# Optimization experiments

Measured on AMD Instinct MI355X. Metric: run time of the kernel, lower is better.

## Reference

```python
import jax, jax.numpy as jnp
import numpy as np

B = 4096
D_FULL, D_T1, D_T2 = 1024, 512, 512
N_SPEC, N_SHARED = 4, 4
HID, OUT = 512, 256


def _expert_params(key, n_experts, d_in):
    k1, k2, k3, k4 = jax.random.split(key, 4)
    s1 = 1.0 / np.sqrt(d_in)
    s2 = 1.0 / np.sqrt(HID)
    return {
        'W1': jax.random.uniform(k1, (n_experts, d_in, HID), jnp.float32, -s1, s1),
        'b1': jax.random.uniform(k2, (n_experts, HID), jnp.float32, -s1, s1),
        'W2': jax.random.uniform(k3, (n_experts, HID, OUT), jnp.float32, -s2, s2),
        'b2': jax.random.uniform(k4, (n_experts, OUT), jnp.float32, -s2, s2),
    }


def setup_inputs() -> dict:
    key = jax.random.key(0)
    ks = jax.random.split(key, 12)
    x_full = jax.random.normal(ks[0], (B, D_FULL), jnp.float32)
    x_task1 = jax.random.normal(ks[1], (B, D_T1), jnp.float32)
    x_task2 = jax.random.normal(ks[2], (B, D_T2), jnp.float32)
    ps = _expert_params(ks[3], N_SHARED, D_FULL)
    p1 = _expert_params(ks[4], N_SPEC, D_T1)
    p2 = _expert_params(ks[5], N_SPEC, D_T2)
    sg = 1.0 / np.sqrt(D_FULL)
    s1 = 1.0 / np.sqrt(D_T1)
    s2 = 1.0 / np.sqrt(D_T2)
    return {
        'x_full': x_full, 'x_task1': x_task1, 'x_task2': x_task2,
        'sh_W1': ps['W1'], 'sh_b1': ps['b1'], 'sh_W2': ps['W2'], 'sh_b2': ps['b2'],
        't1_W1': p1['W1'], 't1_b1': p1['b1'], 't1_W2': p1['W2'], 't1_b2': p1['b2'],
        't2_W1': p2['W1'], 't2_b1': p2['b1'], 't2_W2': p2['W2'], 't2_b2': p2['b2'],
        'gsh_W': jax.random.uniform(ks[6], (D_FULL, 2 * N_SPEC + N_SHARED), jnp.float32, -sg, sg),
        'gsh_b': jax.random.uniform(ks[7], (2 * N_SPEC + N_SHARED,), jnp.float32, -sg, sg),
        'g1_W': jax.random.uniform(ks[8], (D_T1, N_SPEC + N_SHARED), jnp.float32, -s1, s1),
        'g1_b': jax.random.uniform(ks[9], (N_SPEC + N_SHARED,), jnp.float32, -s1, s1),
        'g2_W': jax.random.uniform(ks[10], (D_T2, N_SPEC + N_SHARED), jnp.float32, -s2, s2),
        'g2_b': jax.random.uniform(ks[11], (N_SPEC + N_SHARED,), jnp.float32, -s2, s2),
    }


def _experts(x, W1, b1, W2, b2):
    # x: [B, D]; W1: [E, D, H] -> out [E, B, OUT]
    h = jax.nn.relu(jnp.einsum('bd,edh->ebh', x, W1) + b1[:, None, :])
    return jax.nn.relu(jnp.einsum('ebh,eho->ebo', h, W2) + b2[:, None, :])


def reference(x_full, x_task1, x_task2,
              sh_W1, sh_b1, sh_W2, sh_b2,
              t1_W1, t1_b1, t1_W2, t1_b2,
              t2_W1, t2_b1, t2_W2, t2_b2,
              gsh_W, gsh_b, g1_W, g1_b, g2_W, g2_b):
    eo_shared = _experts(x_full, sh_W1, sh_b1, sh_W2, sh_b2)    # [Es, B, OUT]
    eo_t1 = _experts(x_task1, t1_W1, t1_b1, t1_W2, t1_b2)       # [Et, B, OUT]
    eo_t2 = _experts(x_task2, t2_W1, t2_b1, t2_W2, t2_b2)       # [Et, B, OUT]

    g1 = jax.nn.softmax(x_task1 @ g1_W + g1_b, axis=1)          # [B, Et+Es]
    out1 = jnp.einsum('ebc,be->bc', jnp.concatenate([eo_t1, eo_shared], axis=0), g1)

    g2 = jax.nn.softmax(x_task2 @ g2_W + g2_b, axis=1)
    out2 = jnp.einsum('ebc,be->bc', jnp.concatenate([eo_t2, eo_shared], axis=0), g2)

    gsh = jax.nn.softmax(x_full @ gsh_W + gsh_b, axis=1)        # [B, 2Et+Es]
    out_sh = jnp.einsum('ebc,be->bc', jnp.concatenate([eo_t1, eo_t2, eo_shared], axis=0), gsh)

    return (out_sh, out1, out2)
```

## Files before the change

kernel.cpp:

```cpp
#include <hip/hip_runtime.h>

typedef unsigned short u16;
typedef __attribute__((ext_vector_type(8))) short short8;
typedef __attribute__((ext_vector_type(4))) float f32x4;

#define GL2LDS16(src, dst) __builtin_amdgcn_global_load_lds( \
    (const __attribute__((address_space(1))) void*)(src),    \
    (__attribute__((address_space(3))) void*)(dst), 16, 0, 0)

__device__ __forceinline__ u16 f2bf(float f) {
  union { float f; unsigned u; } v; v.f = f;
  unsigned r = v.u + 0x7fffu + ((v.u >> 16) & 1u);
  return (u16)(r >> 16);
}
__device__ __forceinline__ float bf2f(u16 h) {
  union { unsigned u; float f; } v; v.u = ((unsigned)h) << 16; return v.f;
}

__global__ void k_gates_cvt(const float* __restrict__ xf, const float* __restrict__ x1,
                            const float* __restrict__ x2,
                            const float* __restrict__ gshW, const float* __restrict__ gshB,
                            const float* __restrict__ g1W, const float* __restrict__ g1B,
                            const float* __restrict__ g2W, const float* __restrict__ g2B,
                            u16* __restrict__ xfb, u16* __restrict__ x1b, u16* __restrict__ x2b,
                            float* __restrict__ gsh, float* __restrict__ g1o,
                            float* __restrict__ g2o) {
  const int b = blockIdx.x, lane = threadIdx.x;
  float s[12];
#pragma unroll
  for (int j = 0; j < 12; ++j) s[j] = 0.f;
  {
    const float* xr = xf + (size_t)b * 1024;
    u16* xw = xfb + (size_t)b * 1024;
    for (int k = lane; k < 1024; k += 64) {
      float v = xr[k];
      xw[k] = f2bf(v);
      const float* wr = gshW + (size_t)k * 12;
#pragma unroll
      for (int j = 0; j < 12; ++j) s[j] += v * wr[j];
    }
  }
  float u[8], w[8];
#pragma unroll
  for (int j = 0; j < 8; ++j) { u[j] = 0.f; w[j] = 0.f; }
  {
    const float* xr1 = x1 + (size_t)b * 512;
    const float* xr2 = x2 + (size_t)b * 512;
    u16* xw1 = x1b + (size_t)b * 512;
    u16* xw2 = x2b + (size_t)b * 512;
    for (int k = lane; k < 512; k += 64) {
      float v1 = xr1[k], v2 = xr2[k];
      xw1[k] = f2bf(v1); xw2[k] = f2bf(v2);
      const float* w1r = g1W + (size_t)k * 8;
      const float* w2r = g2W + (size_t)k * 8;
#pragma unroll
      for (int j = 0; j < 8; ++j) { u[j] += v1 * w1r[j]; w[j] += v2 * w2r[j]; }
    }
  }
#pragma unroll
  for (int off = 32; off >= 1; off >>= 1) {
#pragma unroll
    for (int j = 0; j < 12; ++j) s[j] += __shfl_xor(s[j], off, 64);
#pragma unroll
    for (int j = 0; j < 8; ++j) { u[j] += __shfl_xor(u[j], off, 64); w[j] += __shfl_xor(w[j], off, 64); }
  }
  if (lane == 0) {
    float m = -1e30f, tot = 0.f;
#pragma unroll
    for (int j = 0; j < 12; ++j) { s[j] += gshB[j]; m = fmaxf(m, s[j]); }
#pragma unroll
    for (int j = 0; j < 12; ++j) { s[j] = __expf(s[j] - m); tot += s[j]; }
    float inv = 1.f / tot;
#pragma unroll
    for (int j = 0; j < 12; ++j) gsh[(size_t)b * 12 + j] = s[j] * inv;
    m = -1e30f; tot = 0.f;
#pragma unroll
    for (int j = 0; j < 8; ++j) { u[j] += g1B[j]; m = fmaxf(m, u[j]); }
#pragma unroll
    for (int j = 0; j < 8; ++j) { u[j] = __expf(u[j] - m); tot += u[j]; }
    inv = 1.f / tot;
#pragma unroll
    for (int j = 0; j < 8; ++j) g1o[(size_t)b * 8 + j] = u[j] * inv;
    m = -1e30f; tot = 0.f;
#pragma unroll
    for (int j = 0; j < 8; ++j) { w[j] += g2B[j]; m = fmaxf(m, w[j]); }
#pragma unroll
    for (int j = 0; j < 8; ++j) { w[j] = __expf(w[j] - m); tot += w[j]; }
    inv = 1.f / tot;
#pragma unroll
    for (int j = 0; j < 8; ++j) g2o[(size_t)b * 8 + j] = w[j] * inv;
  }
}

struct TD { const float* src; u16* dst; int lgTps; int lgNtx; int R; int C; int tileBase; };
struct TArgs { TD d[6]; };

__global__ void k_transpose_all(TArgs ta) {
  __shared__ float tile[32][33];
  const int x = blockIdx.x;
  int di = 0;
#pragma unroll
  for (int i = 1; i < 6; ++i)
    if (x >= ta.d[i].tileBase) di = i;
  TD d = ta.d[di];
  const int local = x - d.tileBase;
  const int slice = local >> d.lgTps;
  const int ti = local & ((1 << d.lgTps) - 1);
  const int tx = ti & ((1 << d.lgNtx) - 1);
  const int ty = ti >> d.lgNtx;
  const float* src = d.src + (size_t)slice * d.R * d.C;
  u16* dst = d.dst + (size_t)slice * d.R * d.C;
  const int c0 = tx * 32, r0 = ty * 32;
  const int ttx = threadIdx.x, tty = threadIdx.y;
#pragma unroll
  for (int i = tty; i < 32; i += 8)
    tile[i][ttx] = src[(size_t)(r0 + i) * d.C + (c0 + ttx)];
  __syncthreads();
#pragma unroll
  for (int i = tty; i < 32; i += 8)
    dst[(size_t)(c0 + i) * d.R + (r0 + ttx)] = f2bf(tile[ttx][i]);
}

struct GemmDesc {
  const u16* A;
  const u16* BT;
  const float* bias;
  u16* C;
  int K;
  int N;
  int T;
};
struct GemmArgs { GemmDesc d[12]; };

#define BARR __builtin_amdgcn_s_barrier()
#define WAITL0                                                   \
  {                                                              \
    asm volatile("s_waitcnt lgkmcnt(0)" ::: "memory");           \
    __builtin_amdgcn_sched_barrier(0);                           \
  }
#define WAITV0 asm volatile("s_waitcnt vmcnt(0)" ::: "memory")

__global__ __launch_bounds__(512, 4) void k_gemm128(GemmArgs args) {
  __shared__ __align__(16) u16 As[2 * 128 * 32];
  __shared__ __align__(16) u16 Bs[2 * 256 * 32];

  GemmDesc g = args.d[blockIdx.y];
  const int K = g.K, N = g.N, T = g.T;
  const int ntN = N >> 8;
  const int bx = blockIdx.x;
  const int nt = bx & (ntN - 1);
  const int bt = (ntN == 2) ? (bx >> 1) : bx;
  const int row0 = bt << 7;
  const int col0 = nt << 8;

  const int tid = threadIdx.x;
  const int lane = tid & 63;
  const int wid = tid >> 6;
  const int wm = wid & 1;
  const int wn = wid >> 1;
  const int lrow = lane & 15;
  const int lkq = lane >> 4;

  const int csw = (lkq ^ (lrow & 3)) * 16;
  int aoff[4], boff[4];
#pragma unroll
  for (int mi = 0; mi < 4; ++mi) aoff[mi] = (wm * 64 + mi * 16 + lrow) * 64 + csw;
#pragma unroll
  for (int ni = 0; ni < 4; ++ni) boff[ni] = (wn * 64 + ni * 16 + lrow) * 64 + csw;

  const int ar = tid >> 2;
  const int acs = (tid & 3) ^ (ar & 3);
  const u16* aSrc = g.A + (size_t)(row0 + ar) * K + acs * 8;
  const int br0 = tid >> 2;
  const int bc0 = (tid & 3) ^ (br0 & 3);
  const u16* bSrc0 = g.BT + (size_t)(col0 + br0) * K + bc0 * 8;
  const int br1 = 128 + (tid >> 2);
  const int bc1 = (tid & 3) ^ (br1 & 3);
  const u16* bSrc1 = g.BT + (size_t)(col0 + br1) * K + bc1 * 8;

  auto STAGE = [&](int buf, int t) {
    GL2LDS16(aSrc + (size_t)t * 32, &As[buf * 4096 + tid * 8]);
    GL2LDS16(bSrc0 + (size_t)t * 32, &Bs[buf * 8192 + tid * 8]);
    GL2LDS16(bSrc1 + (size_t)t * 32, &Bs[buf * 8192 + 4096 + tid * 8]);
  };

  f32x4 acc[4][4];
#pragma unroll
  for (int m = 0; m < 4; ++m)
#pragma unroll
    for (int n = 0; n < 4; ++n)
      acc[m][n] = (f32x4){0.f, 0.f, 0.f, 0.f};

  STAGE(0, 0);
  WAITV0;
  BARR;

  for (int t = 0; t < T; ++t) {
    const int buf = t & 1;
    const char* Ab = (const char*)As + buf * 8192;
    const char* Bb = (const char*)Bs + buf * 16384;
    short8 a0, a1, b[4];
#pragma unroll
    for (int ni = 0; ni < 4; ++ni) b[ni] = *(const short8*)(Bb + boff[ni]);
    a0 = *(const short8*)(Ab + aoff[0]);
    a1 = *(const short8*)(Ab + aoff[1]);
    if (t + 1 < T) STAGE(buf ^ 1, t + 1);
    WAITL0;
    __builtin_amdgcn_s_setprio(1);
#pragma unroll
    for (int ni = 0; ni < 4; ++ni) {
      acc[0][ni] = __builtin_amdgcn_mfma_f32_16x16x32_bf16(a0, b[ni], acc[0][ni], 0, 0, 0);
      acc[1][ni] = __builtin_amdgcn_mfma_f32_16x16x32_bf16(a1, b[ni], acc[1][ni], 0, 0, 0);
    }
    __builtin_amdgcn_s_setprio(0);
    a0 = *(const short8*)(Ab + aoff[2]);
    a1 = *(const short8*)(Ab + aoff[3]);
    WAITL0;
    __builtin_amdgcn_s_setprio(1);
#pragma unroll
    for (int ni = 0; ni < 4; ++ni) {
      acc[2][ni] = __builtin_amdgcn_mfma_f32_16x16x32_bf16(a0, b[ni], acc[2][ni], 0, 0, 0);
      acc[3][ni] = __builtin_amdgcn_mfma_f32_16x16x32_bf16(a1, b[ni], acc[3][ni], 0, 0, 0);
    }
    __builtin_amdgcn_s_setprio(0);
    WAITV0;
    BARR;
  }

#pragma unroll
  for (int ni = 0; ni < 4; ++ni) {
    const int gc = col0 + wn * 64 + ni * 16 + lrow;
    const float bv = g.bias[gc];
#pragma unroll
    for (int mi = 0; mi < 4; ++mi) {
      const int gr = row0 + wm * 64 + mi * 16 + lkq * 4;
#pragma unroll
      for (int j = 0; j < 4; ++j) {
        float o = fmaxf(acc[mi][ni][j] + bv, 0.f);
        g.C[(size_t)(gr + j) * N + gc] = f2bf(o);
      }
    }
  }
}

__global__ void k_reduce(const u16* __restrict__ OutB, const float* __restrict__ gsh,
                         const float* __restrict__ g1, const float* __restrict__ g2,
                         float* __restrict__ out) {
  int t = blockIdx.x * 256 + threadIdx.x;
  int b = t >> 5;
  int c0 = (t & 31) << 3;
  float wsh[12], w1[8], w2[8];
#pragma unroll
  for (int j = 0; j < 12; ++j) wsh[j] = gsh[(size_t)b * 12 + j];
#pragma unroll
  for (int j = 0; j < 8; ++j) { w1[j] = g1[(size_t)b * 8 + j]; w2[j] = g2[(size_t)b * 8 + j]; }
  float ash[8] = {0, 0, 0, 0, 0, 0, 0, 0};
  float a1[8] = {0, 0, 0, 0, 0, 0, 0, 0};
  float a2[8] = {0, 0, 0, 0, 0, 0, 0, 0};
#pragma unroll
  for (int e = 0; e < 12; ++e) {
    short8 v = *(const short8*)&OutB[((size_t)e * 4096 + b) * 256 + c0];
    float f[8];
#pragma unroll
    for (int i = 0; i < 8; ++i) f[i] = bf2f((u16)v[i]);
#pragma unroll
    for (int i = 0; i < 8; ++i) ash[i] += wsh[e] * f[i];
    if (e < 4) {
#pragma unroll
      for (int i = 0; i < 8; ++i) a1[i] += w1[e] * f[i];
    } else if (e < 8) {
#pragma unroll
      for (int i = 0; i < 8; ++i) a2[i] += w2[e - 4] * f[i];
    } else {
#pragma unroll
      for (int i = 0; i < 8; ++i) a1[i] += w1[e - 4] * f[i];
#pragma unroll
      for (int i = 0; i < 8; ++i) a2[i] += w2[e - 4] * f[i];
    }
  }
  size_t base = (size_t)b * 256 + c0;
  float4* o;
  o = (float4*)(out + base);
  o[0] = make_float4(ash[0], ash[1], ash[2], ash[3]);
  o[1] = make_float4(ash[4], ash[5], ash[6], ash[7]);
  o = (float4*)(out + 4096ull * 256 + base);
  o[0] = make_float4(a1[0], a1[1], a1[2], a1[3]);
  o[1] = make_float4(a1[4], a1[5], a1[6], a1[7]);
  o = (float4*)(out + 2ull * 4096 * 256 + base);
  o[0] = make_float4(a2[0], a2[1], a2[2], a2[3]);
  o[1] = make_float4(a2[4], a2[5], a2[6], a2[7]);
}

extern "C" void kernel_launch(void* const* d_in, const int* in_sizes, int n_in,
                              void* d_out, int out_size, void* d_ws, size_t ws_size,
                              hipStream_t stream) {
  const float* x_full = (const float*)d_in[0];
  const float* x_t1 = (const float*)d_in[1];
  const float* x_t2 = (const float*)d_in[2];
  const float* sh_W1 = (const float*)d_in[3];
  const float* sh_b1 = (const float*)d_in[4];
  const float* sh_W2 = (const float*)d_in[5];
  const float* sh_b2 = (const float*)d_in[6];
  const float* t1_W1 = (const float*)d_in[7];
  const float* t1_b1 = (const float*)d_in[8];
  const float* t1_W2 = (const float*)d_in[9];
  const float* t1_b2 = (const float*)d_in[10];
  const float* t2_W1 = (const float*)d_in[11];
  const float* t2_b1 = (const float*)d_in[12];
  const float* t2_W2 = (const float*)d_in[13];
  const float* t2_b2 = (const float*)d_in[14];
  const float* gsh_W = (const float*)d_in[15];
  const float* gsh_b = (const float*)d_in[16];
  const float* g1_W = (const float*)d_in[17];
  const float* g1_b = (const float*)d_in[18];
  const float* g2_W = (const float*)d_in[19];
  const float* g2_b = (const float*)d_in[20];

  char* ws = (char*)d_ws;
  size_t off = 0;
  auto alloc = [&](size_t bytes) -> void* {
    void* p = ws + off;
    off += (bytes + 255) & ~(size_t)255;
    return p;
  };
  u16* xf_b = (u16*)alloc(4096ull * 1024 * 2);
  u16* x1_b = (u16*)alloc(4096ull * 512 * 2);
  u16* x2_b = (u16*)alloc(4096ull * 512 * 2);
  u16* w1t_t1 = (u16*)alloc(4ull * 512 * 512 * 2);
  u16* w1t_t2 = (u16*)alloc(4ull * 512 * 512 * 2);
  u16* w1t_sh = (u16*)alloc(4ull * 512 * 1024 * 2);
  u16* w2t = (u16*)alloc(12ull * 256 * 512 * 2);
  u16* H = (u16*)alloc(12ull * 4096 * 512 * 2);
  u16* OutB = (u16*)alloc(12ull * 4096 * 256 * 2);
  float* gshv = (float*)alloc(4096ull * 12 * 4);
  float* g1v = (float*)alloc(4096ull * 8 * 4);
  float* g2v = (float*)alloc(4096ull * 8 * 4);

  k_gates_cvt<<<4096, 64, 0, stream>>>(x_full, x_t1, x_t2, gsh_W, gsh_b, g1_W, g1_b, g2_W, g2_b,
                                       xf_b, x1_b, x2_b, gshv, g1v, g2v);

  TArgs ta;
  ta.d[0] = TD{t1_W1, w1t_t1, 8, 4, 512, 512, 0};
  ta.d[1] = TD{t2_W1, w1t_t2, 8, 4, 512, 512, 1024};
  ta.d[2] = TD{sh_W1, w1t_sh, 9, 4, 1024, 512, 2048};
  ta.d[3] = TD{t1_W2, w2t, 7, 3, 512, 256, 4096};
  ta.d[4] = TD{t2_W2, w2t + 4ull * 256 * 512, 7, 3, 512, 256, 4608};
  ta.d[5] = TD{sh_W2, w2t + 8ull * 256 * 512, 7, 3, 512, 256, 5120};
  k_transpose_all<<<5632, dim3(32, 8), 0, stream>>>(ta);

  GemmArgs ga1;
  for (int e = 0; e < 4; ++e) {
    ga1.d[e] = GemmDesc{xf_b, w1t_sh + (size_t)e * 512 * 1024, sh_b1 + e * 512,
                        H + (size_t)(8 + e) * 4096 * 512, 1024, 512, 32};
    ga1.d[4 + e] = GemmDesc{x1_b, w1t_t1 + (size_t)e * 512 * 512, t1_b1 + e * 512,
                            H + (size_t)e * 4096 * 512, 512, 512, 16};
    ga1.d[8 + e] = GemmDesc{x2_b, w1t_t2 + (size_t)e * 512 * 512, t2_b1 + e * 512,
                            H + (size_t)(4 + e) * 4096 * 512, 512, 512, 16};
  }
  k_gemm128<<<dim3(64, 12), 512, 0, stream>>>(ga1);

  GemmArgs ga2;
  for (int e = 0; e < 12; ++e) {
    const float* bias = (e < 4) ? (t1_b2 + e * 256)
                      : (e < 8) ? (t2_b2 + (e - 4) * 256)
                                : (sh_b2 + (e - 8) * 256);
    ga2.d[e] = GemmDesc{H + (size_t)e * 4096 * 512, w2t + (size_t)e * 256 * 512, bias,
                        OutB + (size_t)e * 4096 * 256, 512, 256, 16};
  }
  k_gemm128<<<dim3(32, 12), 512, 0, stream>>>(ga2);

  k_reduce<<<512, 256, 0, stream>>>(OutB, gshv, g1v, g2v, (float*)d_out);
}
```

Measured before the change: 108.0 us.

## Load GEMM A operand directly from global into registers, keep B in LDS

The A tile no longer goes through shared memory. Each wave now reads its A fragments straight from global memory into registers, one step ahead, while B tiles stay double-buffered in LDS through async global-to-LDS loads. The vmcnt waits are made partial so the register prefetch of A overlaps the B staging, the four MFMA row groups are merged into one pass, and the LDS swizzle is changed to XOR with (row>>1). This halves LDS traffic and footprint, at the cost of more global load instructions per wave, since A rows are reread by the four waves sharing wm, and more registers to hold the prefetched A.

```diff
diff --git a/kernel.cpp b/kernel.cpp
--- a/kernel.cpp
+++ b/kernel.cpp
@@ -138,10 +138,13 @@
     asm volatile("s_waitcnt lgkmcnt(0)" ::: "memory");           \
     __builtin_amdgcn_sched_barrier(0);                           \
   }
-#define WAITV0 asm volatile("s_waitcnt vmcnt(0)" ::: "memory")
-
-__global__ __launch_bounds__(512, 4) void k_gemm128(GemmArgs args) {
-  __shared__ __align__(16) u16 As[2 * 128 * 32];
+#define WAITV(N)                                                 \
+  {                                                              \
+    asm volatile("s_waitcnt vmcnt(" #N ")" ::: "memory");        \
+    __builtin_amdgcn_sched_barrier(0);                           \
+  }
+
+__global__ __launch_bounds__(512, 4) void k_gemm_ag(GemmArgs args) {
   __shared__ __align__(16) u16 Bs[2 * 256 * 32];
 
   GemmDesc g = args.d[blockIdx.y];
@@ -161,29 +164,28 @@
   const int lrow = lane & 15;
   const int lkq = lane >> 4;
 
-  const int csw = (lkq ^ (lrow & 3)) * 16;
-  int aoff[4], boff[4];
-#pragma unroll
-  for (int mi = 0; mi < 4; ++mi) aoff[mi] = (wm * 64 + mi * 16 + lrow) * 64 + csw;
+  const int csw = (lkq ^ ((lrow >> 1) & 3)) * 16;
+  int boff[4];
 #pragma unroll
   for (int ni = 0; ni < 4; ++ni) boff[ni] = (wn * 64 + ni * 16 + lrow) * 64 + csw;
 
-  const int ar = tid >> 2;
-  const int acs = (tid & 3) ^ (ar & 3);
-  const u16* aSrc = g.A + (size_t)(row0 + ar) * K + acs * 8;
   const int br0 = tid >> 2;
-  const int bc0 = (tid & 3) ^ (br0 & 3);
+  const int bc0 = (tid & 3) ^ ((br0 >> 1) & 3);
   const u16* bSrc0 = g.BT + (size_t)(col0 + br0) * K + bc0 * 8;
   const int br1 = 128 + (tid >> 2);
-  const int bc1 = (tid & 3) ^ (br1 & 3);
+  const int bc1 = (tid & 3) ^ ((br1 >> 1) & 3);
   const u16* bSrc1 = g.BT + (size_t)(col0 + br1) * K + bc1 * 8;
 
   auto STAGE = [&](int buf, int t) {
-    GL2LDS16(aSrc + (size_t)t * 32, &As[buf * 4096 + tid * 8]);
     GL2LDS16(bSrc0 + (size_t)t * 32, &Bs[buf * 8192 + tid * 8]);
     GL2LDS16(bSrc1 + (size_t)t * 32, &Bs[buf * 8192 + 4096 + tid * 8]);
   };
 
+  const u16* aP[4];
+#pragma unroll
+  for (int mi = 0; mi < 4; ++mi)
+    aP[mi] = g.A + (size_t)(row0 + wm * 64 + mi * 16 + lrow) * K + lkq * 8;
+
   f32x4 acc[4][4];
 #pragma unroll
   for (int m = 0; m < 4; ++m)
@@ -191,39 +193,38 @@
     for (int n = 0; n < 4; ++n)
       acc[m][n] = (f32x4){0.f, 0.f, 0.f, 0.f};
 
+  short8 a[4], b[4];
+
   STAGE(0, 0);
-  WAITV0;
+#pragma unroll
+  for (int mi = 0; mi < 4; ++mi) a[mi] = *(const short8*)(aP[mi]);
+  WAITV(4);
   BARR;
 
   for (int t = 0; t < T; ++t) {
     const int buf = t & 1;
-    const char* Ab = (const char*)As + buf * 8192;
     const char* Bb = (const char*)Bs + buf * 16384;
-    short8 a0, a1, b[4];
+    const bool nl = (t + 1 < T);
 #pragma unroll
     for (int ni = 0; ni < 4; ++ni) b[ni] = *(const short8*)(Bb + boff[ni]);
-    a0 = *(const short8*)(Ab + aoff[0]);
-    a1 = *(const short8*)(Ab + aoff[1]);
-    if (t + 1 < T) STAGE(buf ^ 1, t + 1);
+    if (nl) STAGE(buf ^ 1, t + 1);
     WAITL0;
+    if (nl) { WAITV(2); } else { WAITV(0); }
     __builtin_amdgcn_s_setprio(1);
 #pragma unroll
     for (int ni = 0; ni < 4; ++ni) {
-      acc[0][ni] = __builtin_amdgcn_mfma_f32_16x16x32_bf16(a0, b[ni], acc[0][ni], 0, 0, 0);
-      acc[1][ni] = __builtin_amdgcn_mfma_f32_16x16x32_bf16(a1, b[ni], acc[1][ni], 0, 0, 0);
+      acc[0][ni] = __builtin_amdgcn_mfma_f32_16x16x32_bf16(a[0], b[ni], acc[0][ni], 0, 0, 0);
+      acc[1][ni] = __builtin_amdgcn_mfma_f32_16x16x32_bf16(a[1], b[ni], acc[1][ni], 0, 0, 0);
+      acc[2][ni] = __builtin_amdgcn_mfma_f32_16x16x32_bf16(a[2], b[ni], acc[2][ni], 0, 0, 0);
+      acc[3][ni] = __builtin_amdgcn_mfma_f32_16x16x32_bf16(a[3], b[ni], acc[3][ni], 0, 0, 0);
     }
     __builtin_amdgcn_s_setprio(0);
-    a0 = *(const short8*)(Ab + aoff[2]);
-    a1 = *(const short8*)(Ab + aoff[3]);
-    WAITL0;
-    __builtin_amdgcn_s_setprio(1);
-#pragma unroll
-    for (int ni = 0; ni < 4; ++ni) {
-      acc[2][ni] = __builtin_amdgcn_mfma_f32_16x16x32_bf16(a0, b[ni], acc[2][ni], 0, 0, 0);
-      acc[3][ni] = __builtin_amdgcn_mfma_f32_16x16x32_bf16(a1, b[ni], acc[3][ni], 0, 0, 0);
-    }
-    __builtin_amdgcn_s_setprio(0);
-    WAITV0;
+    if (nl) {
+#pragma unroll
+      for (int mi = 0; mi < 4; ++mi)
+        a[mi] = *(const short8*)(aP[mi] + (size_t)(t + 1) * 32);
+      WAITV(4);
+    }
     BARR;
   }
 
@@ -357,7 +358,7 @@
     ga1.d[8 + e] = GemmDesc{x2_b, w1t_t2 + (size_t)e * 512 * 512, t2_b1 + e * 512,
                             H + (size_t)(4 + e) * 4096 * 512, 512, 512, 16};
   }
-  k_gemm128<<<dim3(64, 12), 512, 0, stream>>>(ga1);
+  k_gemm_ag<<<dim3(64, 12), 512, 0, stream>>>(ga1);
 
   GemmArgs ga2;
   for (int e = 0; e < 12; ++e) {
@@ -367,7 +368,7 @@
     ga2.d[e] = GemmDesc{H + (size_t)e * 4096 * 512, w2t + (size_t)e * 256 * 512, bias,
                         OutB + (size_t)e * 4096 * 256, 512, 256, 16};
   }
-  k_gemm128<<<dim3(32, 12), 512, 0, stream>>>(ga2);
+  k_gemm_ag<<<dim3(32, 12), 512, 0, stream>>>(ga2);
 
   k_reduce<<<512, 256, 0, stream>>>(OutB, gshv, g1v, g2v, (float*)d_out);
 }
```

Result: slower. 160.8 us (+48.9%).

## Fuse gate/convert and transpose kernels; triple-buffer GEMM LDS pipeline

Applied to the files above, without the earlier changes.

Merges the gate-softmax/bf16-convert kernel and the weight transpose kernel into one launch, with 256-thread blocks that handle either a transpose tile or four batch rows. In the GEMM, LDS grows to three stages so loads run two K-steps ahead, using partial vmcnt waits instead of draining all loads each iteration. It also changes the LDS XOR swizzle to use row bits 1-2 to reduce bank conflicts. The larger LDS footprint (72KB) may lower GEMM occupancy against the launch bound of 4 blocks.

```diff
diff --git a/kernel.cpp b/kernel.cpp
--- a/kernel.cpp
+++ b/kernel.cpp
@@ -17,25 +17,55 @@
   union { unsigned u; float f; } v; v.u = ((unsigned)h) << 16; return v.f;
 }
 
-__global__ void k_gates_cvt(const float* __restrict__ xf, const float* __restrict__ x1,
-                            const float* __restrict__ x2,
-                            const float* __restrict__ gshW, const float* __restrict__ gshB,
-                            const float* __restrict__ g1W, const float* __restrict__ g1B,
-                            const float* __restrict__ g2W, const float* __restrict__ g2B,
-                            u16* __restrict__ xfb, u16* __restrict__ x1b, u16* __restrict__ x2b,
-                            float* __restrict__ gsh, float* __restrict__ g1o,
-                            float* __restrict__ g2o) {
-  const int b = blockIdx.x, lane = threadIdx.x;
+struct TD { const float* src; u16* dst; int lgTps; int lgNtx; int R; int C; int tileBase; };
+struct PrepArgs {
+  TD d[6];
+  const float *xf, *x1, *x2;
+  const float *gshW, *gshB, *g1W, *g1B, *g2W, *g2B;
+  u16 *xfb, *x1b, *x2b;
+  float *gsh, *g1o, *g2o;
+};
+
+__global__ void k_prep(PrepArgs pa) {
+  __shared__ float tile[32][33];
+  const int bx = blockIdx.x;
+  const int tid = threadIdx.x;
+  if (bx < 5632) {
+    int di = 0;
+#pragma unroll
+    for (int i = 1; i < 6; ++i)
+      if (bx >= pa.d[i].tileBase) di = i;
+    TD d = pa.d[di];
+    const int local = bx - d.tileBase;
+    const int slice = local >> d.lgTps;
+    const int ti = local & ((1 << d.lgTps) - 1);
+    const int tx = ti & ((1 << d.lgNtx) - 1);
+    const int ty = ti >> d.lgNtx;
+    const float* src = d.src + (size_t)slice * d.R * d.C;
+    u16* dst = d.dst + (size_t)slice * d.R * d.C;
+    const int c0 = tx * 32, r0 = ty * 32;
+    const int ttx = tid & 31, tty = tid >> 5;
+#pragma unroll
+    for (int i = tty; i < 32; i += 8)
+      tile[i][ttx] = src[(size_t)(r0 + i) * d.C + (c0 + ttx)];
+    __syncthreads();
+#pragma unroll
+    for (int i = tty; i < 32; i += 8)
+      dst[(size_t)(c0 + i) * d.R + (r0 + ttx)] = f2bf(tile[ttx][i]);
+    return;
+  }
+  const int b = (bx - 5632) * 4 + (tid >> 6);
+  const int lane = tid & 63;
   float s[12];
 #pragma unroll
   for (int j = 0; j < 12; ++j) s[j] = 0.f;
   {
-    const float* xr = xf + (size_t)b * 1024;
-    u16* xw = xfb + (size_t)b * 1024;
+    const float* xr = pa.xf + (size_t)b * 1024;
+    u16* xw = pa.xfb + (size_t)b * 1024;
     for (int k = lane; k < 1024; k += 64) {
       float v = xr[k];
       xw[k] = f2bf(v);
-      const float* wr = gshW + (size_t)k * 12;
+      const float* wr = pa.gshW + (size_t)k * 12;
 #pragma unroll
       for (int j = 0; j < 12; ++j) s[j] += v * wr[j];
     }
@@ -44,15 +74,15 @@
 #pragma unroll
   for (int j = 0; j < 8; ++j) { u[j] = 0.f; w[j] = 0.f; }
   {
-    const float* xr1 = x1 + (size_t)b * 512;
-    const float* xr2 = x2 + (size_t)b * 512;
-    u16* xw1 = x1b + (size_t)b * 512;
-    u16* xw2 = x2b + (size_t)b * 512;
+    const float* xr1 = pa.x1 + (size_t)b * 512;
+    const float* xr2 = pa.x2 + (size_t)b * 512;
+    u16* xw1 = pa.x1b + (size_t)b * 512;
+    u16* xw2 = pa.x2b + (size_t)b * 512;
     for (int k = lane; k < 512; k += 64) {
       float v1 = xr1[k], v2 = xr2[k];
       xw1[k] = f2bf(v1); xw2[k] = f2bf(v2);
-      const float* w1r = g1W + (size_t)k * 8;
-      const float* w2r = g2W + (size_t)k * 8;
+      const float* w1r = pa.g1W + (size_t)k * 8;
+      const float* w2r = pa.g2W + (size_t)k * 8;
 #pragma unroll
       for (int j = 0; j < 8; ++j) { u[j] += v1 * w1r[j]; w[j] += v2 * w2r[j]; }
     }
@@ -67,58 +97,29 @@
   if (lane == 0) {
     float m = -1e30f, tot = 0.f;
 #pragma unroll
-    for (int j = 0; j < 12; ++j) { s[j] += gshB[j]; m = fmaxf(m, s[j]); }
+    for (int j = 0; j < 12; ++j) { s[j] += pa.gshB[j]; m = fmaxf(m, s[j]); }
 #pragma unroll
     for (int j = 0; j < 12; ++j) { s[j] = __expf(s[j] - m); tot += s[j]; }
     float inv = 1.f / tot;
 #pragma unroll
-    for (int j = 0; j < 12; ++j) gsh[(size_t)b * 12 + j] = s[j] * inv;
+    for (int j = 0; j < 12; ++j) pa.gsh[(size_t)b * 12 + j] = s[j] * inv;
     m = -1e30f; tot = 0.f;
 #pragma unroll
-    for (int j = 0; j < 8; ++j) { u[j] += g1B[j]; m = fmaxf(m, u[j]); }
+    for (int j = 0; j < 8; ++j) { u[j] += pa.g1B[j]; m = fmaxf(m, u[j]); }
 #pragma unroll
     for (int j = 0; j < 8; ++j) { u[j] = __expf(u[j] - m); tot += u[j]; }
     inv = 1.f / tot;
 #pragma unroll
-    for (int j = 0; j < 8; ++j) g1o[(size_t)b * 8 + j] = u[j] * inv;
+    for (int j = 0; j < 8; ++j) pa.g1o[(size_t)b * 8 + j] = u[j] * inv;
     m = -1e30f; tot = 0.f;
 #pragma unroll
-    for (int j = 0; j < 8; ++j) { w[j] += g2B[j]; m = fmaxf(m, w[j]); }
+    for (int j = 0; j < 8; ++j) { w[j] += pa.g2B[j]; m = fmaxf(m, w[j]); }
 #pragma unroll
     for (int j = 0; j < 8; ++j) { w[j] = __expf(w[j] - m); tot += w[j]; }
     inv = 1.f / tot;
 #pragma unroll
-    for (int j = 0; j < 8; ++j) g2o[(size_t)b * 8 + j] = w[j] * inv;
-  }
-}
-
-struct TD { const float* src; u16* dst; int lgTps; int lgNtx; int R; int C; int tileBase; };
-struct TArgs { TD d[6]; };
-
-__global__ void k_transpose_all(TArgs ta) {
-  __shared__ float tile[32][33];
-  const int x = blockIdx.x;
-  int di = 0;
-#pragma unroll
-  for (int i = 1; i < 6; ++i)
-    if (x >= ta.d[i].tileBase) di = i;
-  TD d = ta.d[di];
-  const int local = x - d.tileBase;
-  const int slice = local >> d.lgTps;
-  const int ti = local & ((1 << d.lgTps) - 1);
-  const int tx = ti & ((1 << d.lgNtx) - 1);
-  const int ty = ti >> d.lgNtx;
-  const float* src = d.src + (size_t)slice * d.R * d.C;
-  u16* dst = d.dst + (size_t)slice * d.R * d.C;
-  const int c0 = tx * 32, r0 = ty * 32;
-  const int ttx = threadIdx.x, tty = threadIdx.y;
-#pragma unroll
-  for (int i = tty; i < 32; i += 8)
-    tile[i][ttx] = src[(size_t)(r0 + i) * d.C + (c0 + ttx)];
-  __syncthreads();
-#pragma unroll
-  for (int i = tty; i < 32; i += 8)
-    dst[(size_t)(c0 + i) * d.R + (r0 + ttx)] = f2bf(tile[ttx][i]);
+    for (int j = 0; j < 8; ++j) pa.g2o[(size_t)b * 8 + j] = w[j] * inv;
+  }
 }
 
 struct GemmDesc {
@@ -138,11 +139,16 @@
     asm volatile("s_waitcnt lgkmcnt(0)" ::: "memory");           \
     __builtin_amdgcn_sched_barrier(0);                           \
   }
-#define WAITV0 asm volatile("s_waitcnt vmcnt(0)" ::: "memory")
+#define WAITV(N)                                                 \
+  {                                                              \
+    asm volatile("s_waitcnt vmcnt(" #N ")" ::: "memory");        \
+    __builtin_amdgcn_sched_barrier(0);                           \
+  }
 
 __global__ __launch_bounds__(512, 4) void k_gemm128(GemmArgs args) {
-  __shared__ __align__(16) u16 As[2 * 128 * 32];
-  __shared__ __align__(16) u16 Bs[2 * 256 * 32];
+  __shared__ __align__(16) char lds[73728];
+  u16* As = (u16*)lds;
+  u16* Bs = (u16*)(lds + 24576);
 
   GemmDesc g = args.d[blockIdx.y];
   const int K = g.K, N = g.N, T = g.T;
@@ -161,7 +167,7 @@
   const int lrow = lane & 15;
   const int lkq = lane >> 4;
 
-  const int csw = (lkq ^ (lrow & 3)) * 16;
+  const int csw = (lkq ^ ((lrow >> 1) & 3)) * 16;
   int aoff[4], boff[4];
 #pragma unroll
   for (int mi = 0; mi < 4; ++mi) aoff[mi] = (wm * 64 + mi * 16 + lrow) * 64 + csw;
@@ -169,19 +175,19 @@
   for (int ni = 0; ni < 4; ++ni) boff[ni] = (wn * 64 + ni * 16 + lrow) * 64 + csw;
 
   const int ar = tid >> 2;
-  const int acs = (tid & 3) ^ (ar & 3);
+  const int acs = (tid & 3) ^ ((ar >> 1) & 3);
   const u16* aSrc = g.A + (size_t)(row0 + ar) * K + acs * 8;
   const int br0 = tid >> 2;
-  const int bc0 = (tid & 3) ^ (br0 & 3);
+  const int bc0 = (tid & 3) ^ ((br0 >> 1) & 3);
   const u16* bSrc0 = g.BT + (size_t)(col0 + br0) * K + bc0 * 8;
   const int br1 = 128 + (tid >> 2);
-  const int bc1 = (tid & 3) ^ (br1 & 3);
+  const int bc1 = (tid & 3) ^ ((br1 >> 1) & 3);
   const u16* bSrc1 = g.BT + (size_t)(col0 + br1) * K + bc1 * 8;
 
-  auto STAGE = [&](int buf, int t) {
-    GL2LDS16(aSrc + (size_t)t * 32, &As[buf * 4096 + tid * 8]);
-    GL2LDS16(bSrc0 + (size_t)t * 32, &Bs[buf * 8192 + tid * 8]);
-    GL2LDS16(bSrc1 + (size_t)t * 32, &Bs[buf * 8192 + 4096 + tid * 8]);
+  auto STAGE = [&](int s, int t) {
+    GL2LDS16(aSrc + (size_t)t * 32, &As[s * 4096 + tid * 8]);
+    GL2LDS16(bSrc0 + (size_t)t * 32, &Bs[s * 8192 + tid * 8]);
+    GL2LDS16(bSrc1 + (size_t)t * 32, &Bs[s * 8192 + 4096 + tid * 8]);
   };
 
   f32x4 acc[4][4];
@@ -192,19 +198,20 @@
       acc[m][n] = (f32x4){0.f, 0.f, 0.f, 0.f};
 
   STAGE(0, 0);
-  WAITV0;
+  STAGE(1, 1);
+  WAITV(3);
   BARR;
 
+  int slot = 0, slot2 = 2;
   for (int t = 0; t < T; ++t) {
-    const int buf = t & 1;
-    const char* Ab = (const char*)As + buf * 8192;
-    const char* Bb = (const char*)Bs + buf * 16384;
+    const char* Ab = lds + slot * 8192;
+    const char* Bb = lds + 24576 + slot * 16384;
     short8 a0, a1, b[4];
 #pragma unroll
     for (int ni = 0; ni < 4; ++ni) b[ni] = *(const short8*)(Bb + boff[ni]);
     a0 = *(const short8*)(Ab + aoff[0]);
     a1 = *(const short8*)(Ab + aoff[1]);
-    if (t + 1 < T) STAGE(buf ^ 1, t + 1);
+    if (t + 2 < T) STAGE(slot2, t + 2);
     WAITL0;
     __builtin_amdgcn_s_setprio(1);
 #pragma unroll
@@ -223,8 +230,11 @@
       acc[3][ni] = __builtin_amdgcn_mfma_f32_16x16x32_bf16(a1, b[ni], acc[3][ni], 0, 0, 0);
     }
     __builtin_amdgcn_s_setprio(0);
-    WAITV0;
+    if (t + 2 < T) { WAITV(3); }
+    else if (t + 1 < T) { WAITV(0); }
     BARR;
+    slot = (slot == 2) ? 0 : slot + 1;
+    slot2 = (slot2 == 2) ? 0 : slot2 + 1;
   }
 
 #pragma unroll
@@ -336,17 +346,18 @@
   float* g1v = (float*)alloc(4096ull * 8 * 4);
   float* g2v = (float*)alloc(4096ull * 8 * 4);
 
-  k_gates_cvt<<<4096, 64, 0, stream>>>(x_full, x_t1, x_t2, gsh_W, gsh_b, g1_W, g1_b, g2_W, g2_b,
-                                       xf_b, x1_b, x2_b, gshv, g1v, g2v);
-
-  TArgs ta;
-  ta.d[0] = TD{t1_W1, w1t_t1, 8, 4, 512, 512, 0};
-  ta.d[1] = TD{t2_W1, w1t_t2, 8, 4, 512, 512, 1024};
-  ta.d[2] = TD{sh_W1, w1t_sh, 9, 4, 1024, 512, 2048};
-  ta.d[3] = TD{t1_W2, w2t, 7, 3, 512, 256, 4096};
-  ta.d[4] = TD{t2_W2, w2t + 4ull * 256 * 512, 7, 3, 512, 256, 4608};
-  ta.d[5] = TD{sh_W2, w2t + 8ull * 256 * 512, 7, 3, 512, 256, 5120};
-  k_transpose_all<<<5632, dim3(32, 8), 0, stream>>>(ta);
+  PrepArgs pa;
+  pa.d[0] = TD{t1_W1, w1t_t1, 8, 4, 512, 512, 0};
+  pa.d[1] = TD{t2_W1, w1t_t2, 8, 4, 512, 512, 1024};
+  pa.d[2] = TD{sh_W1, w1t_sh, 9, 4, 1024, 512, 2048};
+  pa.d[3] = TD{t1_W2, w2t, 7, 3, 512, 256, 4096};
+  pa.d[4] = TD{t2_W2, w2t + 4ull * 256 * 512, 7, 3, 512, 256, 4608};
+  pa.d[5] = TD{sh_W2, w2t + 8ull * 256 * 512, 7, 3, 512, 256, 5120};
+  pa.xf = x_full; pa.x1 = x_t1; pa.x2 = x_t2;
+  pa.gshW = gsh_W; pa.gshB = gsh_b; pa.g1W = g1_W; pa.g1B = g1_b; pa.g2W = g2_W; pa.g2B = g2_b;
+  pa.xfb = xf_b; pa.x1b = x1_b; pa.x2b = x2_b;
+  pa.gsh = gshv; pa.g1o = g1v; pa.g2o = g2v;
+  k_prep<<<6656, 256, 0, stream>>>(pa);
 
   GemmArgs ga1;
   for (int e = 0; e < 4; ++e) {
```

Result: slower. 120.9 us (+12.0%).
